# Kernel optimization log

Measured on AMD Instinct MI355X. Metric: run time of the kernel, lower is better.

The kernel has to match this reference:

```python
import jax, jax.numpy as jnp
import numpy as np

B, T, IN, H, L = 128, 2048, 32, 256, 16

def setup_inputs() -> dict:
    key = jax.random.key(0)
    ks = jax.random.split(key, 7)
    s_ih = 1.0 / np.sqrt(IN)
    s_hh = 1.0 / np.sqrt(H)
    return {
        "input_gru": jax.random.normal(ks[0], (B, T, IN), jnp.float32),
        "input_linear": jax.random.normal(ks[1], (B, T, L), jnp.float32),
        "init_hidden": jax.random.normal(ks[2], (B, H), jnp.float32) * 0.1,
        "Wih": jax.random.normal(ks[3], (3 * H, IN), jnp.float32) * s_ih,
        "Whh": jax.random.normal(ks[4], (3 * H, H), jnp.float32) * s_hh,
        "bias": jax.random.normal(ks[5], (3 * H,), jnp.float32) * s_hh,
        "bias_n": jax.random.normal(ks[6], (H,), jnp.float32) * s_hh,
    }

def reference(input_gru, input_linear, init_hidden, Wih, Whh, bias, bias_n):
    # Precompute input-side gate pre-activations for all timesteps: [B,T,3H]
    igates_all = jnp.einsum('bti,gi->btg', input_gru, Wih) + bias
    ig = jnp.moveaxis(igates_all, 1, 0)        # [T,B,3H]
    xl = jnp.moveaxis(input_linear, 1, 0)      # [T,B,L]

    def step(h, inp):
        ig_t, xl_t = inp
        hg = h @ Whh.T                          # [B,3H]
        ir, iz, inew = jnp.split(ig_t, 3, axis=-1)
        hr, hz, hnew = jnp.split(hg, 3, axis=-1)
        r = jax.nn.sigmoid(ir + hr)
        z = jax.nn.sigmoid(iz + hz)             # equinox 'inp' gate
        n = jnp.tanh(inew + r * (hnew + bias_n))
        h_new = n + z * (h - n)                 # equinox GRUCell update
        # dynamic linear readout: params = first L hidden units
        out = jnp.sum(h_new[:, :L] * xl_t, axis=-1, keepdims=True)  # [B,1]
        return h_new, out

    _, outs = jax.lax.scan(step, init_hidden, (ig, xl))  # outs: [T,B,1]
    return jnp.moveaxis(outs, 0, 1)                      # [B,T,1]
```

## Files before the change

kernel.cpp:

```cpp
#include <hip/hip_runtime.h>


typedef _Float16 half8 __attribute__((ext_vector_type(8)));
typedef float float4v __attribute__((ext_vector_type(4)));

#define TT 2048
#define LOG2E 1.44269504088896f

__device__ __forceinline__ float sigm(float x) {
    return __builtin_amdgcn_rcpf(1.f + __builtin_amdgcn_exp2f(-LOG2E * x));
}
__device__ __forceinline__ float tanhf_(float x) {
    float e = __builtin_amdgcn_exp2f(2.f * LOG2E * x);
    return 1.f - 2.f * __builtin_amdgcn_rcpf(e + 1.f);
}

__attribute__((amdgpu_flat_work_group_size(512, 512), amdgpu_waves_per_eu(2, 2)))
__global__ void gru_kernel(const float* __restrict__ xg,
                           const float* __restrict__ xlin,
                           const float* __restrict__ h0,
                           const float* __restrict__ Wih,
                           const float* __restrict__ Whh,
                           const float* __restrict__ bias,
                           const float* __restrict__ biasn,
                           float* __restrict__ out)
{
    __shared__ _Float16 ldsW[24576];
    __shared__ _Float16 ldsWx[24576];
    __shared__ _Float16 ldsH[2][256];

    const int tid  = threadIdx.x;
    const int b    = blockIdx.x;
    const int lane = tid & 63;
    const int w    = tid >> 6;
    const int l15  = lane & 15;
    const int lhi  = lane >> 4;

    half8 Wh[6][7];
#pragma unroll
    for (int nt = 0; nt < 6; ++nt) {
        const int gtile = 2 * w + (nt >> 1) * 16 + (nt & 1);
        const int row = gtile * 16 + l15;
#pragma unroll
        for (int kt = 0; kt < 7; ++kt) {
            const float4v* pp = (const float4v*)(Whh + row * 256 + kt * 32 + lhi * 8);
            float4v u = pp[0], v2 = pp[1];
            half8 hv;
#pragma unroll
            for (int j = 0; j < 4; ++j) { hv[j] = (_Float16)u[j]; hv[4 + j] = (_Float16)v2[j]; }
            Wh[nt][kt] = hv;
        }
    }

    for (int c = tid; c < 3072; c += 512) {
        const int n = c >> 2, qc = c & 3;
        const float* p = Whh + n * 256 + 224 + qc * 8;
        half8 v;
#pragma unroll
        for (int j = 0; j < 8; ++j) v[j] = (_Float16)p[j];
        *(half8*)((char*)ldsW + qc * 12288 + n * 16) = v;
    }
    for (int c = tid; c < 3072; c += 512) {
        const int row = c >> 2, qc = c & 3;
        const float* p = Wih + row * 32 + qc * 8;
        half8 v;
#pragma unroll
        for (int j = 0; j < 8; ++j) v[j] = (_Float16)p[j];
        *(half8*)((char*)ldsWx + (((row >> 4) * 64) + qc * 16 + (row & 15)) * 16) = v;
    }

    float br[2], bz[2], bi[2], bn2[2], hreg[2];
#pragma unroll
    for (int q = 0; q < 2; ++q) {
        const int c = w * 32 + q * 16 + l15;
        br[q]  = bias[c];
        bz[q]  = bias[256 + c];
        bi[q]  = bias[512 + c];
        bn2[q] = biasn[c];
        hreg[q] = h0[b * 256 + c];
    }
    if (tid < 256) ldsH[0][tid] = (_Float16)h0[b * 256 + tid];

    const float* xgb = xg + (size_t)b * TT * 32;
    half8 ax;
    {
        const float4v* px = (const float4v*)(xgb + lhi * 8);
        float4v u = px[0], v2 = px[1];
#pragma unroll
        for (int j = 0; j < 4; ++j) { ax[j] = (_Float16)u[j]; ax[4 + j] = (_Float16)v2[j]; }
    }
    float xlc = 0.f;
    if (w == 0 && lane < 16) xlc = xlin[(size_t)b * TT * 16 + lane];

    __syncthreads();

    const int wb = lhi * 12288 + l15 * 16 + w * 512;
    const float4v zero4 = {0.f, 0.f, 0.f, 0.f};

#pragma clang loop unroll(disable)
    for (int t = 0; t < TT; ++t) {
        const int p  = t & 1;
        const int tn = (t < TT - 1) ? t + 1 : t;

        const float4v* px = (const float4v*)(xgb + (size_t)tn * 32 + lhi * 8);
        float4v xa = px[0], xb2 = px[1];
        float xln = 0.f;
        if (w == 0 && lane < 16) xln = xlin[((size_t)b * TT + tn) * 16 + lane];

        float4v acc[6];
        float xn2[2];
#pragma unroll
        for (int nt = 0; nt < 6; ++nt) {
            const int gtile = 2 * w + (nt >> 1) * 16 + (nt & 1);
            half8 wx = *(const half8*)((const char*)ldsWx + gtile * 1024 + lhi * 256 + l15 * 16);
            float4v xq = __builtin_amdgcn_mfma_f32_16x16x32_f16(ax, wx, zero4, 0, 0, 0);
            if (nt >= 4) { xn2[nt - 4] = xq[0]; acc[nt] = zero4; }
            else         { acc[nt] = xq; }
        }
#pragma unroll
        for (int kt = 0; kt < 8; ++kt) {
            half8 a = ((const half8*)ldsH[p])[kt * 4 + lhi];
#pragma unroll
            for (int nt = 0; nt < 6; ++nt) {
                half8 bb;
                if (kt < 7) bb = Wh[nt][kt];
                else        bb = *(const half8*)((const char*)ldsW + wb
                                      + (nt >> 1) * 4096 + (nt & 1) * 256);
                acc[nt] = __builtin_amdgcn_mfma_f32_16x16x32_f16(a, bb, acc[nt], 0, 0, 0);
            }
        }

#pragma unroll
        for (int q = 0; q < 2; ++q) {
            float r = sigm(acc[q][0] + br[q]);
            float z = sigm(acc[2 + q][0] + bz[q]);
            float n = tanhf_(xn2[q] + bi[q] + r * (acc[4 + q][0] + bn2[q]));
            float hnew = n + z * (hreg[q] - n);
            hreg[q] = hnew;
            if (lane < 16) ldsH[p ^ 1][w * 32 + q * 16 + l15] = (_Float16)hnew;
        }

        if (w == 0) {
            float v = hreg[0] * xlc;
            v += __shfl_xor(v, 8, 16);
            v += __shfl_xor(v, 4, 16);
            v += __shfl_xor(v, 2, 16);
            v += __shfl_xor(v, 1, 16);
            if (lane == 0) out[(size_t)b * TT + t] = v;
        }

#pragma unroll
        for (int j = 0; j < 4; ++j) { ax[j] = (_Float16)xa[j]; ax[4 + j] = (_Float16)xb2[j]; }
        xlc = xln;
        __syncthreads();
    }
}

extern "C" void kernel_launch(void* const* d_in, const int* in_sizes, int n_in,
                              void* d_out, int out_size, void* d_ws, size_t ws_size,
                              hipStream_t stream) {
    const float* xg    = (const float*)d_in[0];
    const float* xlin  = (const float*)d_in[1];
    const float* h0    = (const float*)d_in[2];
    const float* Wih   = (const float*)d_in[3];
    const float* Whh   = (const float*)d_in[4];
    const float* bias  = (const float*)d_in[5];
    const float* biasn = (const float*)d_in[6];
    float* out = (float*)d_out;

    gru_kernel<<<128, 512, 0, stream>>>(xg, xlin, h0, Wih, Whh, bias, biasn, out);
}
```

Measured before the change: 2.512 ms.

## Split GRU gate tiles across 16 waves per block instead of 8

Doubles the workgroup to 1024 threads so each wave owns one 16-column slice per gate (3 tiles) instead of two (6 tiles). This halves per-wave MFMA chain length and register-resident Whh fragments, shortening the serial per-timestep critical path. The cost is more waves contending for the per-step block barrier and LDS broadcast reads of h, and register pressure must fit 1024-thread launch bounds.

```diff
diff --git a/kernel.cpp b/kernel.cpp
--- a/kernel.cpp
+++ b/kernel.cpp
@@ -15,7 +15,7 @@
     return 1.f - 2.f * __builtin_amdgcn_rcpf(e + 1.f);
 }
 
-__attribute__((amdgpu_flat_work_group_size(512, 512), amdgpu_waves_per_eu(2, 2)))
+__launch_bounds__(1024)
 __global__ void gru_kernel(const float* __restrict__ xg,
                            const float* __restrict__ xlin,
                            const float* __restrict__ h0,
@@ -36,11 +36,10 @@
     const int l15  = lane & 15;
     const int lhi  = lane >> 4;
 
-    half8 Wh[6][7];
+    half8 Wh[3][7];
 #pragma unroll
-    for (int nt = 0; nt < 6; ++nt) {
-        const int gtile = 2 * w + (nt >> 1) * 16 + (nt & 1);
-        const int row = gtile * 16 + l15;
+    for (int nt = 0; nt < 3; ++nt) {
+        const int row = (nt * 16 + w) * 16 + l15;
 #pragma unroll
         for (int kt = 0; kt < 7; ++kt) {
             const float4v* pp = (const float4v*)(Whh + row * 256 + kt * 32 + lhi * 8);
@@ -52,7 +51,7 @@
         }
     }
 
-    for (int c = tid; c < 3072; c += 512) {
+    for (int c = tid; c < 3072; c += 1024) {
         const int n = c >> 2, qc = c & 3;
         const float* p = Whh + n * 256 + 224 + qc * 8;
         half8 v;
@@ -60,7 +59,7 @@
         for (int j = 0; j < 8; ++j) v[j] = (_Float16)p[j];
         *(half8*)((char*)ldsW + qc * 12288 + n * 16) = v;
     }
-    for (int c = tid; c < 3072; c += 512) {
+    for (int c = tid; c < 3072; c += 1024) {
         const int row = c >> 2, qc = c & 3;
         const float* p = Wih + row * 32 + qc * 8;
         half8 v;
@@ -69,16 +68,12 @@
         *(half8*)((char*)ldsWx + (((row >> 4) * 64) + qc * 16 + (row & 15)) * 16) = v;
     }
 
-    float br[2], bz[2], bi[2], bn2[2], hreg[2];
-#pragma unroll
-    for (int q = 0; q < 2; ++q) {
-        const int c = w * 32 + q * 16 + l15;
-        br[q]  = bias[c];
-        bz[q]  = bias[256 + c];
-        bi[q]  = bias[512 + c];
-        bn2[q] = biasn[c];
-        hreg[q] = h0[b * 256 + c];
-    }
+    const int col = w * 16 + l15;
+    const float b_r = bias[col];
+    const float b_z = bias[256 + col];
+    const float b_i = bias[512 + col];
+    const float b_n = biasn[col];
+    float hreg = h0[b * 256 + col];
     if (tid < 256) ldsH[0][tid] = (_Float16)h0[b * 256 + tid];
 
     const float* xgb = xg + (size_t)b * TT * 32;
@@ -94,7 +89,8 @@
 
     __syncthreads();
 
-    const int wb = lhi * 12288 + l15 * 16 + w * 512;
+    const int wxb = w * 1024 + lhi * 256 + l15 * 16;
+    const int wb  = lhi * 12288 + w * 256 + l15 * 16;
     const float4v zero4 = {0.f, 0.f, 0.f, 0.f};
 
 #pragma clang loop unroll(disable)
@@ -107,41 +103,38 @@
         float xln = 0.f;
         if (w == 0 && lane < 16) xln = xlin[((size_t)b * TT + tn) * 16 + lane];
 
-        float4v acc[6];
-        float xn2[2];
+        float4v acc[3];
+        float xn;
 #pragma unroll
-        for (int nt = 0; nt < 6; ++nt) {
-            const int gtile = 2 * w + (nt >> 1) * 16 + (nt & 1);
-            half8 wx = *(const half8*)((const char*)ldsWx + gtile * 1024 + lhi * 256 + l15 * 16);
+        for (int nt = 0; nt < 3; ++nt) {
+            half8 wx = *(const half8*)((const char*)ldsWx + wxb + nt * 16384);
             float4v xq = __builtin_amdgcn_mfma_f32_16x16x32_f16(ax, wx, zero4, 0, 0, 0);
-            if (nt >= 4) { xn2[nt - 4] = xq[0]; acc[nt] = zero4; }
+            if (nt == 2) { xn = xq[0]; acc[2] = zero4; }
             else         { acc[nt] = xq; }
         }
 #pragma unroll
         for (int kt = 0; kt < 8; ++kt) {
             half8 a = ((const half8*)ldsH[p])[kt * 4 + lhi];
 #pragma unroll
-            for (int nt = 0; nt < 6; ++nt) {
+            for (int nt = 0; nt < 3; ++nt) {
                 half8 bb;
                 if (kt < 7) bb = Wh[nt][kt];
-                else        bb = *(const half8*)((const char*)ldsW + wb
-                                      + (nt >> 1) * 4096 + (nt & 1) * 256);
+                else        bb = *(const half8*)((const char*)ldsW + wb + nt * 4096);
                 acc[nt] = __builtin_amdgcn_mfma_f32_16x16x32_f16(a, bb, acc[nt], 0, 0, 0);
             }
         }
 
-#pragma unroll
-        for (int q = 0; q < 2; ++q) {
-            float r = sigm(acc[q][0] + br[q]);
-            float z = sigm(acc[2 + q][0] + bz[q]);
-            float n = tanhf_(xn2[q] + bi[q] + r * (acc[4 + q][0] + bn2[q]));
-            float hnew = n + z * (hreg[q] - n);
-            hreg[q] = hnew;
-            if (lane < 16) ldsH[p ^ 1][w * 32 + q * 16 + l15] = (_Float16)hnew;
+        {
+            float r = sigm(acc[0][0] + b_r);
+            float z = sigm(acc[1][0] + b_z);
+            float n = tanhf_(xn + b_i + r * (acc[2][0] + b_n));
+            float hnew = n + z * (hreg - n);
+            hreg = hnew;
+            if (lane < 16) ldsH[p ^ 1][col] = (_Float16)hnew;
         }
 
         if (w == 0) {
-            float v = hreg[0] * xlc;
+            float v = hreg * xlc;
             v += __shfl_xor(v, 8, 16);
             v += __shfl_xor(v, 4, 16);
             v += __shfl_xor(v, 2, 16);
@@ -168,5 +161,5 @@
     const float* biasn = (const float*)d_in[6];
     float* out = (float*)d_out;
 
-    gru_kernel<<<128, 512, 0, stream>>>(xg, xlin, h0, Wih, Whh, bias, biasn, out);
+    gru_kernel<<<128, 1024, 0, stream>>>(xg, xlin, h0, Wih, Whh, bias, biasn, out);
 }
```

Result: slower. 3.002 ms (+19.5%).
